# Kernel optimization log

Measured on AMD Instinct MI355X. Metric: run time of the kernel, lower is better.

The kernel has to match this reference:

```python
import jax, jax.numpy as jnp
import numpy as np

NUM_HEADS = 16
NUM_KV_HEADS = 4
HEAD_DIM = 128
EPS = 1e-6


def _rotate_half(x):
    x1, x2 = jnp.split(x, 2, axis=-1)
    return jnp.concatenate((-x2, x1), axis=-1)


def _rms_norm(x, w):
    var = jnp.mean(x * x, axis=-1, keepdims=True)
    return x * jax.lax.rsqrt(var + EPS) * w


def setup_inputs() -> dict:
    key = jax.random.key(0)
    ks = jax.random.split(key, 6)
    B, S, H = 2, 2048, 2048
    hidden_states = jax.random.normal(ks[0], (B, S, H), dtype=jnp.float32)
    # real RoPE tables (HF-style: freqs tiled twice along last dim)
    inv_freq = 1.0 / (10000.0 ** (np.arange(0, HEAD_DIM, 2, dtype=np.float32) / HEAD_DIM))
    pos = np.arange(S, dtype=np.float32)
    ang = np.concatenate([pos[:, None] * inv_freq[None, :]] * 2, axis=-1)  # [S, head_dim]
    cos = jnp.broadcast_to(jnp.cos(ang)[None], (B, S, HEAD_DIM)).astype(jnp.float32)
    sin = jnp.broadcast_to(jnp.sin(ang)[None], (B, S, HEAD_DIM)).astype(jnp.float32)
    sc = 0.02
    Wq = jax.random.normal(ks[1], (NUM_HEADS * HEAD_DIM, H), dtype=jnp.float32) * sc
    Wk = jax.random.normal(ks[2], (NUM_KV_HEADS * HEAD_DIM, H), dtype=jnp.float32) * sc
    Wv = jax.random.normal(ks[3], (NUM_KV_HEADS * HEAD_DIM, H), dtype=jnp.float32) * sc
    Wo = jax.random.normal(ks[4], (H, NUM_HEADS * HEAD_DIM), dtype=jnp.float32) * sc
    q_norm_w = jnp.ones((HEAD_DIM,), dtype=jnp.float32)
    k_norm_w = jnp.ones((HEAD_DIM,), dtype=jnp.float32)
    return {"hidden_states": hidden_states, "cos": cos, "sin": sin,
            "Wq": Wq, "Wk": Wk, "Wv": Wv, "Wo": Wo,
            "q_norm_w": q_norm_w, "k_norm_w": k_norm_w}


def reference(hidden_states, cos, sin, Wq, Wk, Wv, Wo, q_norm_w, k_norm_w):
    B, S, H = hidden_states.shape
    groups = NUM_HEADS // NUM_KV_HEADS
    # projections (Linear: x @ W^T), then [B, h, S, d]
    q = (hidden_states @ Wq.T).reshape(B, S, NUM_HEADS, HEAD_DIM).transpose(0, 2, 1, 3)
    k = (hidden_states @ Wk.T).reshape(B, S, NUM_KV_HEADS, HEAD_DIM).transpose(0, 2, 1, 3)
    v = (hidden_states @ Wv.T).reshape(B, S, NUM_KV_HEADS, HEAD_DIM).transpose(0, 2, 1, 3)
    # per-head RMSNorm
    q = _rms_norm(q, q_norm_w)
    k = _rms_norm(k, k_norm_w)
    # RoPE, cos/sin broadcast over heads (unsqueeze_dim=1)
    c = cos[:, None, :, :]
    s = sin[:, None, :, :]
    q = q * c + _rotate_half(q) * s
    k = k * c + _rotate_half(k) * s
    # GQA: expand kv heads
    k = jnp.repeat(k, groups, axis=1)
    v = jnp.repeat(v, groups, axis=1)
    scale = 1.0 / jnp.sqrt(jnp.float32(HEAD_DIM))
    scores = jnp.einsum('bhqd,bhkd->bhqk', q, k) * scale
    attn = jax.nn.softmax(scores, axis=-1)
    out = jnp.einsum('bhqk,bhkd->bhqd', attn, v)
    out = out.transpose(0, 2, 1, 3).reshape(B, S, NUM_HEADS * HEAD_DIM)
    return out @ Wo.T
```

## Files before the change

### kernel.cpp

```cpp
#include <hip/hip_runtime.h>
#include <hip/hip_bf16.h>
#include <stdint.h>

typedef __attribute__((ext_vector_type(8))) short short8;
typedef __attribute__((ext_vector_type(4))) float floatx4;
typedef __attribute__((ext_vector_type(16))) float floatx16;

#define MFMA16(a, b, c) __builtin_amdgcn_mfma_f32_16x16x32_bf16(a, b, c, 0, 0, 0)
#define MFMA32(a, b, c) __builtin_amdgcn_mfma_f32_32x32x16_bf16(a, b, c, 0, 0, 0)

static __device__ __forceinline__ void gload_lds16(const __hip_bfloat16* g, __hip_bfloat16* l) {
  __builtin_amdgcn_global_load_lds(
      (const __attribute__((address_space(1))) void*)g,
      (__attribute__((address_space(3))) void*)l,
      16, 0, 0);
}

__global__ __launch_bounds__(256)
void f2bf_all(const float* __restrict__ h, const float* __restrict__ wq,
              const float* __restrict__ wk, const float* __restrict__ wv,
              const float* __restrict__ wo, __hip_bfloat16* __restrict__ hb,
              __hip_bfloat16* __restrict__ wqkv, __hip_bfloat16* __restrict__ wob) {
  const int blk = blockIdx.x;
  const float* src;
  __hip_bfloat16* dst;
  int off;
  if (blk < 8192)       { src = h;  dst = hb;                          off = blk; }
  else if (blk < 12288) { src = wq; dst = wqkv;                        off = blk - 8192; }
  else if (blk < 13312) { src = wk; dst = wqkv + (size_t)2048 * 2048;  off = blk - 12288; }
  else if (blk < 14336) { src = wv; dst = wqkv + (size_t)2560 * 2048;  off = blk - 13312; }
  else                  { src = wo; dst = wob;                         off = blk - 14336; }
  const int i = off * 1024 + threadIdx.x * 4;
  const float4 v = *(const float4*)(src + i);
  __hip_bfloat16 t[4] = {__float2bfloat16(v.x), __float2bfloat16(v.y),
                         __float2bfloat16(v.z), __float2bfloat16(v.w)};
  *(short4*)(dst + i) = *(const short4*)t;
}

template <typename OUT_T>
__global__ __launch_bounds__(256)
void gemm_bt(const __hip_bfloat16* __restrict__ A, const __hip_bfloat16* __restrict__ Bt,
             OUT_T* __restrict__ C, int M, int N, int K) {
  __shared__ __hip_bfloat16 As[2][128 * 32];
  __shared__ __hip_bfloat16 Bs[2][128 * 32];
  const int tid = threadIdx.x;
  const int wid = tid >> 6, lane = tid & 63;
  const int lg = lane >> 4, lr = lane & 15;
  const int wr = wid >> 1, wc = wid & 1;
  const int m0 = blockIdx.x * 128, n0 = blockIdx.y * 128;
  const int nk = K >> 5;

  floatx4 acc[4][4];
#pragma unroll
  for (int mi = 0; mi < 4; ++mi)
#pragma unroll
    for (int ni = 0; ni < 4; ++ni) acc[mi][ni] = (floatx4)(0.0f);

  auto stage = [&](int buf, int kt) {
    const int k0 = kt << 5;
#pragma unroll
    for (int i = 0; i < 2; ++i) {
      const int e = (i * 256 + tid) * 8;
      const int row = e >> 5, col = e & 31;
      gload_lds16(A + (size_t)(m0 + row) * K + k0 + col, &As[buf][e]);
    }
#pragma unroll
    for (int i = 0; i < 2; ++i) {
      const int e = (i * 256 + tid) * 8;
      const int row = e >> 5, col = e & 31;
      gload_lds16(Bt + (size_t)(n0 + row) * K + k0 + col, &Bs[buf][e]);
    }
  };

  stage(0, 0);
  __syncthreads();

  for (int kt = 0; kt < nk; ++kt) {
    const int cur = kt & 1;
    if (kt + 1 < nk) stage(cur ^ 1, kt + 1);
    short8 af[4], bfr[4];
#pragma unroll
    for (int mi = 0; mi < 4; ++mi)
      af[mi] = *(const short8*)&As[cur][(wr * 64 + mi * 16 + lr) * 32 + lg * 8];
#pragma unroll
    for (int ni = 0; ni < 4; ++ni)
      bfr[ni] = *(const short8*)&Bs[cur][(wc * 64 + ni * 16 + lr) * 32 + lg * 8];
#pragma unroll
    for (int mi = 0; mi < 4; ++mi)
#pragma unroll
      for (int ni = 0; ni < 4; ++ni) acc[mi][ni] = MFMA16(af[mi], bfr[ni], acc[mi][ni]);
    __syncthreads();
  }

#pragma unroll
  for (int mi = 0; mi < 4; ++mi)
#pragma unroll
    for (int ni = 0; ni < 4; ++ni) {
      const int row = m0 + wr * 64 + mi * 16 + lg * 4;
      const int col = n0 + wc * 64 + ni * 16 + lr;
#pragma unroll
      for (int r = 0; r < 4; ++r) {
        C[(size_t)(row + r) * N + col] = (OUT_T)acc[mi][ni][r];
      }
    }
}

__global__ __launch_bounds__(256)
void normrope(const __hip_bfloat16* __restrict__ qkv, const float* __restrict__ cosb,
              const float* __restrict__ sinb, const float* __restrict__ qw,
              const float* __restrict__ kw, __hip_bfloat16* __restrict__ Q,
              __hip_bfloat16* __restrict__ K) {
  const int m = blockIdx.x;
  const int b = m >> 11, s = m & 2047;
  const int wid = threadIdx.x >> 6, lane = threadIdx.x & 63;
  const size_t qkvrow = (size_t)m * 3072;
  const float c1 = cosb[(size_t)m * 128 + lane], s1 = sinb[(size_t)m * 128 + lane];
  const float c2 = cosb[(size_t)m * 128 + lane + 64], s2 = sinb[(size_t)m * 128 + lane + 64];
  for (int h = wid * 5; h < wid * 5 + 5; ++h) {
    const float x1 = __bfloat162float(qkv[qkvrow + h * 128 + lane]);
    const float x2 = __bfloat162float(qkv[qkvrow + h * 128 + lane + 64]);
    float ss = x1 * x1 + x2 * x2;
    ss += __shfl_xor(ss, 1);  ss += __shfl_xor(ss, 2);  ss += __shfl_xor(ss, 4);
    ss += __shfl_xor(ss, 8);  ss += __shfl_xor(ss, 16); ss += __shfl_xor(ss, 32);
    const float rs = rsqrtf(ss * (1.0f / 128.0f) + 1e-6f);
    const float* w = (h < 16) ? qw : kw;
    const float n1 = x1 * rs * w[lane], n2 = x2 * rs * w[lane + 64];
    const float o1 = n1 * c1 - n2 * s1;
    const float o2 = n2 * c2 + n1 * s2;
    if (h < 16) {
      const size_t base = ((size_t)(b * 16 + h) * 2048 + s) * 128;
      Q[base + lane] = __float2bfloat16(o1);
      Q[base + lane + 64] = __float2bfloat16(o2);
    } else {
      const size_t base = ((size_t)(b * 4 + h - 16) * 2048 + s) * 128;
      K[base + lane] = __float2bfloat16(o1);
      K[base + lane + 64] = __float2bfloat16(o2);
    }
  }
}

__global__ __launch_bounds__(256)
void kblock(const __hip_bfloat16* __restrict__ K, __hip_bfloat16* __restrict__ Kb2) {
  const int z = blockIdx.y;
  const int t = blockIdx.x * 4 + (threadIdx.x >> 6);
  const int kv = threadIdx.x & 63;
  const short* src = (const short*)K + (size_t)z * 262144 + t * 8192;
  short* dst = (short*)Kb2 + (size_t)z * 262144 + t * 8192;
#pragma unroll
  for (int cd = 0; cd < 16; ++cd) {
    const short8 v = *(const short8*)&src[kv * 128 + cd * 8];
    *(short8*)&dst[cd * 512 + kv * 8] = v;
  }
}

__global__ __launch_bounds__(256)
void vtrans2(const __hip_bfloat16* __restrict__ qkv, __hip_bfloat16* __restrict__ Vt2) {
  __shared__ short L[64 * 65];
  const int tid = threadIdx.x;
  const int t = blockIdx.x, d0 = blockIdx.y * 64, z = blockIdx.z;
  const int b = z >> 2, hkv = z & 3;
  const int s0 = t * 64;
#pragma unroll
  for (int i = 0; i < 2; ++i) {
    const int slot = i * 256 + tid;
    const int srow = slot >> 3, c8 = (slot & 7) * 8;
    const short8 v = *(const short8*)((const short*)qkv +
        (size_t)(b * 2048 + s0 + srow) * 3072 + 2560 + hkv * 128 + d0 + c8);
#pragma unroll
    for (int j = 0; j < 8; ++j) L[(c8 + j) * 65 + srow] = v[j];
  }
  __syncthreads();
  short* dst = (short*)Vt2 + (size_t)z * 262144 + t * 8192;
#pragma unroll
  for (int i = 0; i < 2; ++i) {
    const int slot = i * 256 + tid;
    const int drow = slot >> 3, sc8 = (slot & 7) * 8;
    short8 o;
#pragma unroll
    for (int j = 0; j < 8; ++j) {
      const int p = sc8 + j;
      const int pb = p & 31;
      const int phys = (p & ~31) | ((pb & 3) + ((pb >> 2) & 1) * 8 + ((pb >> 3) & 1) * 4 + (pb & 16));
      o[j] = L[drow * 65 + phys];
    }
    *(short8*)&dst[(sc8 >> 3) * 1024 + (d0 + drow) * 8] = o;
  }
}

__global__ __launch_bounds__(256, 2)
void fattn(const __hip_bfloat16* __restrict__ Qg, const __hip_bfloat16* __restrict__ Kb2,
           const __hip_bfloat16* __restrict__ Vt2, __hip_bfloat16* __restrict__ Og) {
  __shared__ short SMEM[40960];

  const int tid = threadIdx.x, wid = tid >> 6, lane = tid & 63;
  const int l31 = lane & 31, hi = lane >> 5;
  const int qt = blockIdx.x, bh = blockIdx.y;
  const int b = bh >> 4, h = bh & 15, hkv = h >> 2;
  const int z = b * 4 + hkv;
  const int q0w = qt * 128 + wid * 32;

  const __hip_bfloat16* Qrow = Qg + ((size_t)((b * 16 + h) * 2048 + q0w + l31)) * 128;
  short8 qf2[8];
#pragma unroll
  for (int ks = 0; ks < 8; ++ks) qf2[ks] = *(const short8*)(Qrow + ks * 16 + hi * 8);

  const short* Kbase = (const short*)Kb2 + (size_t)z * 262144;
  const short* Vbase = (const short*)Vt2 + (size_t)z * 262144;

  auto stageK = [&](int buf, int t) {
    const short* ks = Kbase + t * 8192 + wid * 2048 + lane * 8;
    short* kd = &SMEM[buf * 8192 + wid * 2048];
#pragma unroll
    for (int i = 0; i < 4; ++i)
      gload_lds16((const __hip_bfloat16*)(ks + i * 512), (__hip_bfloat16*)(kd + i * 512));
  };
  auto stageV = [&](int slot, int t) {
    const short* vs = Vbase + t * 8192 + wid * 2048 + lane * 8;
    short* vd = &SMEM[16384 + slot * 8192 + wid * 2048];
#pragma unroll
    for (int i = 0; i < 4; ++i)
      gload_lds16((const __hip_bfloat16*)(vs + i * 512), (__hip_bfloat16*)(vd + i * 512));
  };

  floatx16 oacc[4];
#pragma unroll
  for (int dblk = 0; dblk < 4; ++dblk) oacc[dblk] = (floatx16)(0.0f);
  float la0 = 0.0f, la1 = 0.0f;

  const float SC2 = 0.12753102497113446f;
  const float OFF2 = 17.31234049066756f;

  int pkA[2][8], pkB[2][8];

  auto doQK = [&](int kbuf, floatx16 (&st)[2]) {
    const short* Kt = &SMEM[kbuf * 8192];
    st[0] = (floatx16)(0.0f);
    st[1] = (floatx16)(0.0f);
    __builtin_amdgcn_s_setprio(1);
#pragma unroll
    for (int ks = 0; ks < 8; ++ks) {
      const short8 kf0 = *(const short8*)&Kt[(ks * 2 + hi) * 512 + l31 * 8];
      const short8 kf1 = *(const short8*)&Kt[(ks * 2 + hi) * 512 + 256 + l31 * 8];
      st[0] = MFMA32(kf0, qf2[ks], st[0]);
      st[1] = MFMA32(kf1, qf2[ks], st[1]);
    }
    __builtin_amdgcn_s_setprio(0);
  };
  auto doExp = [&](const floatx16 (&st)[2], int (&pk)[2][8]) {
#pragma unroll
    for (int kvblk = 0; kvblk < 2; ++kvblk)
#pragma unroll
      for (int m = 0; m < 8; ++m) {
        const float e0 = exp2f(fmaf(st[kvblk][2 * m], SC2, -OFF2));
        const float e1 = exp2f(fmaf(st[kvblk][2 * m + 1], SC2, -OFF2));
        if (m & 1) la1 += e0 + e1; else la0 += e0 + e1;
        asm("v_cvt_pk_bf16_f32 %0, %1, %2" : "=v"(pk[kvblk][m]) : "v"(e0), "v"(e1));
      }
  };
  auto doPV = [&](int vslot, const int (&pk)[2][8]) {
    const short* Vt = &SMEM[16384 + vslot * 8192];
#pragma unroll
    for (int kvblk = 0; kvblk < 2; ++kvblk) {
#pragma unroll
      for (int s = 0; s < 2; ++s) {
        union { int i[4]; short8 s8; } u;
        u.i[0] = pk[kvblk][4 * s + 0];
        u.i[1] = pk[kvblk][4 * s + 1];
        u.i[2] = pk[kvblk][4 * s + 2];
        u.i[3] = pk[kvblk][4 * s + 3];
        const short8 pB = u.s8;
        const int c = kvblk * 4 + s * 2 + hi;
        __builtin_amdgcn_s_setprio(1);
#pragma unroll
        for (int dblk = 0; dblk < 4; ++dblk) {
          const short8 vf = *(const short8*)&Vt[c * 1024 + dblk * 256 + l31 * 8];
          oacc[dblk] = MFMA32(vf, pB, oacc[dblk]);
        }
        __builtin_amdgcn_s_setprio(0);
      }
    }
  };

  int vs_stage = 2, vs_pv = 0;
  auto body = [&](int (&pkPrev)[2][8], int (&pkCur)[2][8], int u) {
    if (u + 1 < 32) {
      stageK((u + 1) & 1, u + 1);
      stageV(vs_stage, u + 1);
    }
    floatx16 st[2];
    doQK(u & 1, st);
    doPV(vs_pv, pkPrev);
    doExp(st, pkCur);
    vs_stage = (vs_stage == 2) ? 0 : vs_stage + 1;
    vs_pv = (vs_pv == 2) ? 0 : vs_pv + 1;
    asm volatile("s_waitcnt vmcnt(0)" ::: "memory");
    __builtin_amdgcn_s_barrier();
    __builtin_amdgcn_sched_barrier(0);
  };

  stageK(0, 0);
  stageV(0, 0);
  asm volatile("s_waitcnt vmcnt(0)" ::: "memory");
  __builtin_amdgcn_s_barrier();
  __builtin_amdgcn_sched_barrier(0);
  {
    stageK(1, 1);
    stageV(1, 1);
    floatx16 st[2];
    doQK(0, st);
    doExp(st, pkA);
    asm volatile("s_waitcnt vmcnt(0)" ::: "memory");
    __builtin_amdgcn_s_barrier();
    __builtin_amdgcn_sched_barrier(0);
  }

  for (int u = 1; u < 31; u += 2) {
    body(pkA, pkB, u);
    body(pkB, pkA, u + 1);
  }
  body(pkA, pkB, 31);
  doPV(vs_pv, pkB);

  const float l_own = la0 + la1;
  const float l = l_own + __shfl_xor(l_own, 32);
  const float inv = 1.0f / l;
  short* tw = &SMEM[wid * 4352];
#pragma unroll
  for (int dblk = 0; dblk < 4; ++dblk)
#pragma unroll
    for (int a = 0; a < 4; ++a) {
      __hip_bfloat16 o4[4];
#pragma unroll
      for (int r = 0; r < 4; ++r) o4[r] = __float2bfloat16(oacc[dblk][4 * a + r] * inv);
      *(short4*)&tw[l31 * 136 + dblk * 32 + a * 8 + hi * 4] = *(const short4*)o4;
    }
  __hip_bfloat16* orow =
      Og + ((size_t)(b * 2048 + q0w + (lane >> 1))) * 2048 + h * 128 + (lane & 1) * 64;
  const short* trow = &tw[(lane >> 1) * 136 + (lane & 1) * 64];
#pragma unroll
  for (int c = 0; c < 8; ++c) {
    *(short8*)(orow + c * 8) = *(const short8*)(trow + c * 8);
  }
}

extern "C" void kernel_launch(void* const* d_in, const int* in_sizes, int n_in,
                              void* d_out, int out_size, void* d_ws, size_t ws_size,
                              hipStream_t stream) {
  const float* hidden = (const float*)d_in[0];
  const float* cosb = (const float*)d_in[1];
  const float* sinb = (const float*)d_in[2];
  const float* Wq = (const float*)d_in[3];
  const float* Wk = (const float*)d_in[4];
  const float* Wv = (const float*)d_in[5];
  const float* Wo = (const float*)d_in[6];
  const float* qw = (const float*)d_in[7];
  const float* kw = (const float*)d_in[8];

  char* ws = (char*)d_ws;
  __hip_bfloat16* hidden_bf = (__hip_bfloat16*)ws; ws += (size_t)4096 * 2048 * 2;
  __hip_bfloat16* wqkv = (__hip_bfloat16*)ws;      ws += (size_t)3072 * 2048 * 2;
  __hip_bfloat16* wo_bf = (__hip_bfloat16*)ws;     ws += (size_t)2048 * 2048 * 2;
  __hip_bfloat16* qkv = (__hip_bfloat16*)ws;       ws += (size_t)4096 * 3072 * 2;
  __hip_bfloat16* Qb = (__hip_bfloat16*)ws;        ws += (size_t)2 * 16 * 2048 * 128 * 2;
  __hip_bfloat16* Kb = (__hip_bfloat16*)ws;        ws += (size_t)2 * 4 * 2048 * 128 * 2;
  __hip_bfloat16* Kb2 = (__hip_bfloat16*)ws;       ws += (size_t)2 * 4 * 2048 * 128 * 2;
  __hip_bfloat16* attn = (__hip_bfloat16*)ws;      ws += (size_t)4096 * 2048 * 2;
  __hip_bfloat16* Vt2 = wqkv;

  f2bf_all<<<18432, 256, 0, stream>>>(hidden, Wq, Wk, Wv, Wo, hidden_bf, wqkv, wo_bf);

  gemm_bt<__hip_bfloat16><<<dim3(32, 24), 256, 0, stream>>>(hidden_bf, wqkv, qkv, 4096, 3072, 2048);
  normrope<<<4096, 256, 0, stream>>>(qkv, cosb, sinb, qw, kw, Qb, Kb);
  kblock<<<dim3(8, 8), 256, 0, stream>>>(Kb, Kb2);
  vtrans2<<<dim3(32, 2, 8), 256, 0, stream>>>(qkv, Vt2);
  fattn<<<dim3(16, 32), 256, 0, stream>>>(Qb, Kb2, Vt2, attn);
  gemm_bt<float><<<dim3(32, 16), 256, 0, stream>>>(attn, wo_bf, (float*)d_out, 4096, 2048, 2048);
}
```

Measured before the change: 234.7 us.

## Fuse K blocking into normrope, fold softmax scale into Q, widen attention blocks

Result: slower. 356.1 us (+51.7%).

```diff
diff --git a/kernel.cpp b/kernel.cpp
--- a/kernel.cpp
+++ b/kernel.cpp
@@ -109,13 +109,14 @@
 void normrope(const __hip_bfloat16* __restrict__ qkv, const float* __restrict__ cosb,
               const float* __restrict__ sinb, const float* __restrict__ qw,
               const float* __restrict__ kw, __hip_bfloat16* __restrict__ Q,
-              __hip_bfloat16* __restrict__ K) {
+              __hip_bfloat16* __restrict__ Kblk) {
   const int m = blockIdx.x;
   const int b = m >> 11, s = m & 2047;
   const int wid = threadIdx.x >> 6, lane = threadIdx.x & 63;
   const size_t qkvrow = (size_t)m * 3072;
   const float c1 = cosb[(size_t)m * 128 + lane], s1 = sinb[(size_t)m * 128 + lane];
   const float c2 = cosb[(size_t)m * 128 + lane + 64], s2 = sinb[(size_t)m * 128 + lane + 64];
+  const float QS = 0.12753102497113446f;
   for (int h = wid * 5; h < wid * 5 + 5; ++h) {
     const float x1 = __bfloat162float(qkv[qkvrow + h * 128 + lane]);
     const float x2 = __bfloat162float(qkv[qkvrow + h * 128 + lane + 64]);
@@ -129,27 +130,16 @@
     const float o2 = n2 * c2 + n1 * s2;
     if (h < 16) {
       const size_t base = ((size_t)(b * 16 + h) * 2048 + s) * 128;
-      Q[base + lane] = __float2bfloat16(o1);
-      Q[base + lane + 64] = __float2bfloat16(o2);
+      Q[base + lane] = __float2bfloat16(o1 * QS);
+      Q[base + lane + 64] = __float2bfloat16(o2 * QS);
     } else {
-      const size_t base = ((size_t)(b * 4 + h - 16) * 2048 + s) * 128;
-      K[base + lane] = __float2bfloat16(o1);
-      K[base + lane + 64] = __float2bfloat16(o2);
-    }
-  }
-}
-
-__global__ __launch_bounds__(256)
-void kblock(const __hip_bfloat16* __restrict__ K, __hip_bfloat16* __restrict__ Kb2) {
-  const int z = blockIdx.y;
-  const int t = blockIdx.x * 4 + (threadIdx.x >> 6);
-  const int kv = threadIdx.x & 63;
-  const short* src = (const short*)K + (size_t)z * 262144 + t * 8192;
-  short* dst = (short*)Kb2 + (size_t)z * 262144 + t * 8192;
-#pragma unroll
-  for (int cd = 0; cd < 16; ++cd) {
-    const short8 v = *(const short8*)&src[kv * 128 + cd * 8];
-    *(short8*)&dst[cd * 512 + kv * 8] = v;
+      const int z = b * 4 + (h - 16);
+      const int t = s >> 6, kv = s & 63;
+      const size_t base =
+          (size_t)z * 262144 + t * 8192 + (lane >> 3) * 512 + kv * 8 + (lane & 7);
+      Kblk[base] = __float2bfloat16(o1);
+      Kblk[base + 4096] = __float2bfloat16(o2);
+    }
   }
 }
 
@@ -187,17 +177,17 @@
   }
 }
 
-__global__ __launch_bounds__(256, 2)
+__global__ __launch_bounds__(512, 4)
 void fattn(const __hip_bfloat16* __restrict__ Qg, const __hip_bfloat16* __restrict__ Kb2,
            const __hip_bfloat16* __restrict__ Vt2, __hip_bfloat16* __restrict__ Og) {
-  __shared__ short SMEM[40960];
+  __shared__ short SMEM[34816];
 
   const int tid = threadIdx.x, wid = tid >> 6, lane = tid & 63;
   const int l31 = lane & 31, hi = lane >> 5;
   const int qt = blockIdx.x, bh = blockIdx.y;
   const int b = bh >> 4, h = bh & 15, hkv = h >> 2;
   const int z = b * 4 + hkv;
-  const int q0w = qt * 128 + wid * 32;
+  const int q0w = qt * 256 + wid * 32;
 
   const __hip_bfloat16* Qrow = Qg + ((size_t)((b * 16 + h) * 2048 + q0w + l31)) * 128;
   short8 qf2[8];
@@ -206,17 +196,18 @@
 
   const short* Kbase = (const short*)Kb2 + (size_t)z * 262144;
   const short* Vbase = (const short*)Vt2 + (size_t)z * 262144;
+  const int wq = wid & 3;
 
   auto stageK = [&](int buf, int t) {
-    const short* ks = Kbase + t * 8192 + wid * 2048 + lane * 8;
-    short* kd = &SMEM[buf * 8192 + wid * 2048];
+    const short* ks = Kbase + t * 8192 + wq * 2048 + lane * 8;
+    short* kd = &SMEM[buf * 8192 + wq * 2048];
 #pragma unroll
     for (int i = 0; i < 4; ++i)
       gload_lds16((const __hip_bfloat16*)(ks + i * 512), (__hip_bfloat16*)(kd + i * 512));
   };
-  auto stageV = [&](int slot, int t) {
-    const short* vs = Vbase + t * 8192 + wid * 2048 + lane * 8;
-    short* vd = &SMEM[16384 + slot * 8192 + wid * 2048];
+  auto stageV = [&](int buf, int t) {
+    const short* vs = Vbase + t * 8192 + wq * 2048 + lane * 8;
+    short* vd = &SMEM[16384 + buf * 8192 + wq * 2048];
 #pragma unroll
     for (int i = 0; i < 4; ++i)
       gload_lds16((const __hip_bfloat16*)(vs + i * 512), (__hip_bfloat16*)(vd + i * 512));
@@ -226,9 +217,6 @@
 #pragma unroll
   for (int dblk = 0; dblk < 4; ++dblk) oacc[dblk] = (floatx16)(0.0f);
   float la0 = 0.0f, la1 = 0.0f;
-
-  const float SC2 = 0.12753102497113446f;
-  const float OFF2 = 17.31234049066756f;
 
   int pkA[2][8], pkB[2][8];
 
@@ -251,14 +239,14 @@
     for (int kvblk = 0; kvblk < 2; ++kvblk)
 #pragma unroll
       for (int m = 0; m < 8; ++m) {
-        const float e0 = exp2f(fmaf(st[kvblk][2 * m], SC2, -OFF2));
-        const float e1 = exp2f(fmaf(st[kvblk][2 * m + 1], SC2, -OFF2));
+        const float e0 = exp2f(st[kvblk][2 * m]);
+        const float e1 = exp2f(st[kvblk][2 * m + 1]);
         if (m & 1) la1 += e0 + e1; else la0 += e0 + e1;
         asm("v_cvt_pk_bf16_f32 %0, %1, %2" : "=v"(pk[kvblk][m]) : "v"(e0), "v"(e1));
       }
   };
-  auto doPV = [&](int vslot, const int (&pk)[2][8]) {
-    const short* Vt = &SMEM[16384 + vslot * 8192];
+  auto doPV = [&](int vbuf, const int (&pk)[2][8]) {
+    const short* Vt = &SMEM[16384 + vbuf * 8192];
 #pragma unroll
     for (int kvblk = 0; kvblk < 2; ++kvblk) {
 #pragma unroll
@@ -281,31 +269,25 @@
     }
   };
 
-  int vs_stage = 2, vs_pv = 0;
   auto body = [&](int (&pkPrev)[2][8], int (&pkCur)[2][8], int u) {
-    if (u + 1 < 32) {
-      stageK((u + 1) & 1, u + 1);
-      stageV(vs_stage, u + 1);
-    }
+    if (wid < 4) { if (u + 1 < 32) stageK((u + 1) & 1, u + 1); }
+    else stageV(u & 1, u);
     floatx16 st[2];
     doQK(u & 1, st);
-    doPV(vs_pv, pkPrev);
+    doPV((u - 1) & 1, pkPrev);
     doExp(st, pkCur);
-    vs_stage = (vs_stage == 2) ? 0 : vs_stage + 1;
-    vs_pv = (vs_pv == 2) ? 0 : vs_pv + 1;
     asm volatile("s_waitcnt vmcnt(0)" ::: "memory");
     __builtin_amdgcn_s_barrier();
     __builtin_amdgcn_sched_barrier(0);
   };
 
-  stageK(0, 0);
-  stageV(0, 0);
+  if (wid < 4) stageK(0, 0);
   asm volatile("s_waitcnt vmcnt(0)" ::: "memory");
   __builtin_amdgcn_s_barrier();
   __builtin_amdgcn_sched_barrier(0);
   {
-    stageK(1, 1);
-    stageV(1, 1);
+    if (wid < 4) stageK(1, 1);
+    else stageV(0, 0);
     floatx16 st[2];
     doQK(0, st);
     doExp(st, pkA);
@@ -319,7 +301,10 @@
     body(pkB, pkA, u + 1);
   }
   body(pkA, pkB, 31);
-  doPV(vs_pv, pkB);
+  doPV(1, pkB);
+
+  asm volatile("s_waitcnt lgkmcnt(0)" ::: "memory");
+  __builtin_amdgcn_s_barrier();
 
   const float l_own = la0 + la1;
   const float l = l_own + __shfl_xor(l_own, 32);
@@ -362,17 +347,15 @@
   __hip_bfloat16* wo_bf = (__hip_bfloat16*)ws;     ws += (size_t)2048 * 2048 * 2;
   __hip_bfloat16* qkv = (__hip_bfloat16*)ws;       ws += (size_t)4096 * 3072 * 2;
   __hip_bfloat16* Qb = (__hip_bfloat16*)ws;        ws += (size_t)2 * 16 * 2048 * 128 * 2;
-  __hip_bfloat16* Kb = (__hip_bfloat16*)ws;        ws += (size_t)2 * 4 * 2048 * 128 * 2;
-  __hip_bfloat16* Kb2 = (__hip_bfloat16*)ws;       ws += (size_t)2 * 4 * 2048 * 128 * 2;
+  __hip_bfloat16* Kblk = (__hip_bfloat16*)ws;      ws += (size_t)2 * 4 * 2048 * 128 * 2;
   __hip_bfloat16* attn = (__hip_bfloat16*)ws;      ws += (size_t)4096 * 2048 * 2;
   __hip_bfloat16* Vt2 = wqkv;
 
   f2bf_all<<<18432, 256, 0, stream>>>(hidden, Wq, Wk, Wv, Wo, hidden_bf, wqkv, wo_bf);
 
   gemm_bt<__hip_bfloat16><<<dim3(32, 24), 256, 0, stream>>>(hidden_bf, wqkv, qkv, 4096, 3072, 2048);
-  normrope<<<4096, 256, 0, stream>>>(qkv, cosb, sinb, qw, kw, Qb, Kb);
-  kblock<<<dim3(8, 8), 256, 0, stream>>>(Kb, Kb2);
+  normrope<<<4096, 256, 0, stream>>>(qkv, cosb, sinb, qw, kw, Qb, Kblk);
   vtrans2<<<dim3(32, 2, 8), 256, 0, stream>>>(qkv, Vt2);
-  fattn<<<dim3(16, 32), 256, 0, stream>>>(Qb, Kb2, Vt2, attn);
+  fattn<<<dim3(8, 32), 512, 0, stream>>>(Qb, Kblk, Vt2, attn);
   gemm_bt<float><<<dim3(32, 16), 256, 0, stream>>>(attn, wo_bf, (float*)d_out, 4096, 2048, 2048);
 }
```
